# Kernel tuning notes

Measured on AMD Instinct MI355X. Metric: run time of the kernel, lower is better.

The kernel has to match this reference:

```python
import jax, jax.numpy as jnp
import numpy as np

NUM_HEADS = 8
DIM_HEAD = 40
SCALE = DIM_HEAD ** (-1.0 / 4.0)  # applied to q AND k, net 1/sqrt(dim_head)


def setup_inputs() -> dict:
    key = jax.random.key(0)
    ks = jax.random.split(key, 7)
    B, T, Dq = 16, 4096, 320
    S, Dc = 77, 768
    inner = NUM_HEADS * DIM_HEAD  # 320
    return {
        "x": jax.random.normal(ks[0], (B, T, Dq), jnp.float32),
        "context": jax.random.normal(ks[1], (B, S, Dc), jnp.float32),
        "Wq": jax.random.normal(ks[2], (Dq, inner), jnp.float32) * 0.02,
        "Wk": jax.random.normal(ks[3], (Dc, inner), jnp.float32) * 0.02,
        "Wv": jax.random.normal(ks[4], (Dc, inner), jnp.float32) * 0.02,
        "Wo": jax.random.normal(ks[5], (inner, Dq), jnp.float32) * 0.02,
        "bo": jnp.zeros((Dq,), jnp.float32),
    }


def reference(x, context, Wq, Wk, Wv, Wo, bo):
    B, T, _ = x.shape
    S = context.shape[1]
    H, C = NUM_HEADS, DIM_HEAD
    # projections; scale applied to q and k separately (dim_head^-1/4 each)
    q = (x @ Wq * SCALE).reshape(B, T, H, C)        # [B,T,H,C]
    k = (context @ Wk * SCALE).reshape(B, S, H, C)  # [B,S,H,C]
    v = (context @ Wv).reshape(B, S, H, C)          # [B,S,H,C]
    scores = jnp.einsum("bthc,bshc->bhts", q, k)    # [B,H,T,S]
    attn = jax.nn.softmax(scores, axis=-1)
    out = jnp.einsum("bhts,bshc->bthc", attn, v).reshape(B, T, H * C)
    return out @ Wo + bo
```

## Files before the change

### kernel.cpp

```cpp
#include <hip/hip_runtime.h>
#include <math.h>


#define NUM_HEADS 8
#define DIM_HEAD 40
#define INNER 320
#define DQ 320
#define DC 768
#define SEQ_T 4096
#define SEQ_S 77
#define BATCH 16
#define M_TOTAL (BATCH * SEQ_T)
#define MKV 1232
#define MKV_PAD 1280
#define SCALE 0.39763536438352531f

typedef __attribute__((ext_vector_type(8))) short short8;
typedef __attribute__((ext_vector_type(4))) float floatx4;

__device__ __forceinline__ unsigned short f2bf(float f) {
  unsigned u = __float_as_uint(f);
  u += 0x7FFFu + ((u >> 16) & 1u);
  return (unsigned short)(u >> 16);
}

#define CTXBLKS (MKV_PAD * DC / 8 / 256)
__global__ __launch_bounds__(256) void convert_ctx_kernel(
    const float* __restrict__ ctx, unsigned short* __restrict__ ctxb) {
  size_t t = (size_t)blockIdx.x * 256 + threadIdx.x;
  int row = (int)(t / (DC / 8)), col = (int)(t % (DC / 8)) * 8;
  int4 pk = make_int4(0, 0, 0, 0);
  if (row < MKV) {
    const float* p = &ctx[(size_t)row * DC + col];
    float4 a = *(const float4*)p, b = *(const float4*)(p + 4);
    pk.x = (int)(f2bf(a.x) | ((unsigned)f2bf(a.y) << 16));
    pk.y = (int)(f2bf(a.z) | ((unsigned)f2bf(a.w) << 16));
    pk.z = (int)(f2bf(b.x) | ((unsigned)f2bf(b.y) << 16));
    pk.w = (int)(f2bf(b.z) | ((unsigned)f2bf(b.w) << 16));
  }
  *(int4*)&ctxb[(size_t)row * DC + col] = pk;
}

__global__ __launch_bounds__(256) void transpose_w_kernel(
    const float* __restrict__ Wq, const float* __restrict__ Wo,
    const float* __restrict__ Wk, const float* __restrict__ Wv,
    unsigned short* __restrict__ WqT, unsigned short* __restrict__ WoT,
    unsigned short* __restrict__ WkvT) {
  const int z = blockIdx.z;
  const float* W; unsigned short* WT; int KD; float scl = 1.0f;
  if (z == 0)      { W = Wq; WT = WqT;  KD = 320; }
  else if (z == 1) { W = Wo; WT = WoT;  KD = 320; }
  else if (z == 2) { W = Wk; WT = WkvT; KD = DC; scl = SCALE; }
  else             { W = Wv; WT = WkvT + (size_t)INNER * DC; KD = DC; }
  const int k0 = blockIdx.x * 32;
  if (k0 >= KD) return;
  const int n0 = blockIdx.y * 32;
  __shared__ float tile[32][33];
  int tx = threadIdx.x & 31, ty = threadIdx.x >> 5;
  #pragma unroll
  for (int r = 0; r < 4; ++r)
    tile[ty + r * 8][tx] = W[(size_t)(k0 + ty + r * 8) * 320 + n0 + tx];
  __syncthreads();
  #pragma unroll
  for (int r = 0; r < 4; ++r)
    WT[(size_t)(n0 + ty + r * 8) * KD + k0 + tx] = f2bf(tile[tx][ty + r * 8] * scl);
}

#define GBM 128
#define GBN 160
#define GBK 64

template <bool OUT_BF16, int K, int CN>
__global__ __launch_bounds__(256) void gemm_mfma_kernel(
    const unsigned short* __restrict__ A, const unsigned short* __restrict__ B,
    void* __restrict__ C, const float* __restrict__ bias, float scale) {
  __shared__ __align__(16) unsigned short As[GBM * GBK];
  __shared__ __align__(16) unsigned short Bs[GBN * GBK];
  const int tid = threadIdx.x;
  const int lane = tid & 63, wave = tid >> 6;
  const int wm = (wave & 1) * 64, wn = (wave >> 1) * 80;
  const int lrow = lane & 15, quad = lane >> 4;
  const unsigned short* Ab = A + (size_t)blockIdx.x * GBM * K;
  const unsigned short* Bb = B + (size_t)blockIdx.y * GBN * K;

  floatx4 acc[4][5];
  #pragma unroll
  for (int i = 0; i < 4; ++i)
    #pragma unroll
    for (int j = 0; j < 5; ++j) acc[i][j] = (floatx4){0.f, 0.f, 0.f, 0.f};

  for (int kb = 0; kb < K / GBK; ++kb) {
    const int k0 = kb * GBK;
    #pragma unroll
    for (int rnd = 0; rnd < 4; ++rnd) {
      int off = rnd * 4096 + tid * 16;
      int m = off >> 7, cl = (off >> 4) & 7, cg = cl ^ (m & 7);
      __builtin_amdgcn_global_load_lds(
          (const __attribute__((address_space(1))) void*)(Ab + (size_t)m * K + k0 + cg * 8),
          (__attribute__((address_space(3))) void*)((char*)As + off), 16, 0, 0);
    }
    #pragma unroll
    for (int rnd = 0; rnd < 5; ++rnd) {
      int off = rnd * 4096 + tid * 16;
      int n = off >> 7, cl = (off >> 4) & 7, cg = cl ^ (n & 7);
      __builtin_amdgcn_global_load_lds(
          (const __attribute__((address_space(1))) void*)(Bb + (size_t)n * K + k0 + cg * 8),
          (__attribute__((address_space(3))) void*)((char*)Bs + off), 16, 0, 0);
    }
    __syncthreads();
    #pragma unroll
    for (int ks = 0; ks < 2; ++ks) {
      short8 fa[4], fb[5];
      #pragma unroll
      for (int i = 0; i < 4; ++i) {
        int m = wm + i * 16 + lrow;
        int cl = (ks * 4 + quad) ^ (m & 7);
        fa[i] = *(const short8*)&As[m * GBK + cl * 8];
      }
      #pragma unroll
      for (int j = 0; j < 5; ++j) {
        int n = wn + j * 16 + lrow;
        int cl = (ks * 4 + quad) ^ (n & 7);
        fb[j] = *(const short8*)&Bs[n * GBK + cl * 8];
      }
      #pragma unroll
      for (int i = 0; i < 4; ++i)
        #pragma unroll
        for (int j = 0; j < 5; ++j)
          acc[i][j] = __builtin_amdgcn_mfma_f32_16x16x32_bf16(fa[i], fb[j], acc[i][j], 0, 0, 0);
    }
    __syncthreads();
  }
  #pragma unroll
  for (int i = 0; i < 4; ++i)
    #pragma unroll
    for (int j = 0; j < 5; ++j) {
      int n = blockIdx.y * GBN + wn + j * 16 + lrow;
      float bv = bias ? bias[n] : 0.f;
      #pragma unroll
      for (int r = 0; r < 4; ++r) {
        size_t m = (size_t)blockIdx.x * GBM + wm + i * 16 + quad * 4 + r;
        float val = acc[i][j][r] * scale + bv;
        if (OUT_BF16) ((unsigned short*)C)[m * CN + n] = f2bf(val);
        else          ((float*)C)[m * CN + n] = val;
      }
    }
}

__global__ __launch_bounds__(256) void prep_kv_kernel(
    const float* __restrict__ kvw, unsigned short* __restrict__ kvp) {
  const int b = blockIdx.x >> 3, h = blockIdx.x & 7;
  unsigned short* dst = kvp + (size_t)blockIdx.x * 8192;
  const float* kvb = kvw + (size_t)b * SEQ_S * 640;
  for (int i = threadIdx.x; i < 3200; i += 256) {
    int s = i / 40, c = i % 40;
    unsigned short v = 0;
    if (s < SEQ_S) v = f2bf(kvb[(size_t)s * 640 + h * DIM_HEAD + c]);
    dst[i] = v;
  }
  for (int i = threadIdx.x; i < 4992; i += 256) {
    int c = i / 104, s = i % 104;
    unsigned short v = 0;
    if (s < SEQ_S && c < DIM_HEAD)
      v = f2bf(kvb[(size_t)s * 640 + 320 + h * DIM_HEAD + c]);
    dst[3200 + i] = v;
  }
}

#define QS_STRIDE 328
#define LDS_STAGE 41984

__global__ __launch_bounds__(512) void fused_attn_kernel(
    const float* __restrict__ x, const unsigned short* __restrict__ WqT,
    const unsigned short* __restrict__ kvp, const unsigned short* __restrict__ WoT,
    const float* __restrict__ bo, float* __restrict__ out) {
  __shared__ __align__(16) unsigned short lds[70656];
  unsigned short* qs = lds;
  unsigned short* As = lds + LDS_STAGE;
  unsigned short* Bs = lds + LDS_STAGE + 8192;
  const int tid = threadIdx.x;
  const int lane = tid & 63, wave = tid >> 6;
  const int lrow = lane & 15, quad = lane >> 4;
  const int b = blockIdx.x >> 5;
  const int t0 = (blockIdx.x & 31) * 128;
  const int wm = (wave & 1) * 64, wn = (wave >> 1) * 80;

  {
    const float* xb = x + ((size_t)b * SEQ_T + t0) * DQ;
    floatx4 acc[4][5];
    #pragma unroll
    for (int i = 0; i < 4; ++i)
      #pragma unroll
      for (int j = 0; j < 5; ++j) acc[i][j] = (floatx4){0.f, 0.f, 0.f, 0.f};
    for (int kb = 0; kb < 5; ++kb) {
      const int k0 = kb * 64;
      #pragma unroll
      for (int rnd = 0; rnd < 2; ++rnd) {
        int off = rnd * 8192 + tid * 16;
        int m = off >> 7, cl = (off >> 4) & 7, cg = cl ^ (m & 7);
        const float* src = xb + (size_t)m * DQ + k0 + cg * 8;
        float4 a = *(const float4*)src, c = *(const float4*)(src + 4);
        short8 pk;
        pk[0] = (short)f2bf(a.x); pk[1] = (short)f2bf(a.y);
        pk[2] = (short)f2bf(a.z); pk[3] = (short)f2bf(a.w);
        pk[4] = (short)f2bf(c.x); pk[5] = (short)f2bf(c.y);
        pk[6] = (short)f2bf(c.z); pk[7] = (short)f2bf(c.w);
        *(short8*)((char*)As + off) = pk;
      }
      #pragma unroll
      for (int rnd = 0; rnd < 5; ++rnd) {
        int off = rnd * 8192 + tid * 16;
        int n = off >> 7, cl = (off >> 4) & 7, cg = cl ^ (n & 7);
        __builtin_amdgcn_global_load_lds(
            (const __attribute__((address_space(1))) void*)(WqT + (size_t)n * 320 + k0 + cg * 8),
            (__attribute__((address_space(3))) void*)((char*)Bs + off), 16, 0, 0);
      }
      __syncthreads();
      #pragma unroll
      for (int ks = 0; ks < 2; ++ks) {
        short8 fa[4], fb[5];
        #pragma unroll
        for (int i = 0; i < 4; ++i) {
          int m = wm + i * 16 + lrow;
          int cl = (ks * 4 + quad) ^ (m & 7);
          fa[i] = *(const short8*)&As[m * 64 + cl * 8];
        }
        #pragma unroll
        for (int j = 0; j < 5; ++j) {
          int n = wn + j * 16 + lrow;
          int cl = (ks * 4 + quad) ^ (n & 7);
          fb[j] = *(const short8*)&Bs[n * 64 + cl * 8];
        }
        #pragma unroll
        for (int i = 0; i < 4; ++i)
          #pragma unroll
          for (int j = 0; j < 5; ++j)
            acc[i][j] = __builtin_amdgcn_mfma_f32_16x16x32_bf16(fa[i], fb[j], acc[i][j], 0, 0, 0);
      }
      __syncthreads();
    }
    #pragma unroll
    for (int i = 0; i < 4; ++i)
      #pragma unroll
      for (int j = 0; j < 5; ++j)
        #pragma unroll
        for (int r = 0; r < 4; ++r)
          qs[(wm + i * 16 + quad * 4 + r) * QS_STRIDE + wn + j * 16 + lrow] =
              f2bf(acc[i][j][r] * SCALE);
  }
  __syncthreads();

  {
    unsigned short* Kb = lds + LDS_STAGE;
    unsigned short* Vt = lds + LDS_STAGE + 3200;
    unsigned short* Pw = lds + LDS_STAGE + 8192 + wave * 1664;
    const short8 zero8 = {0, 0, 0, 0, 0, 0, 0, 0};
    for (int h = 0; h < NUM_HEADS; ++h) {
      const unsigned short* kvbh = kvp + (size_t)(b * NUM_HEADS + h) * 8192;
      #pragma unroll
      for (int rnd = 0; rnd < 2; ++rnd) {
        int off = rnd * 8192 + tid * 16;
        __builtin_amdgcn_global_load_lds(
            (const __attribute__((address_space(1))) void*)((const char*)kvbh + off),
            (__attribute__((address_space(3))) void*)((char*)Kb + off), 16, 0, 0);
      }
      __syncthreads();
      const int qrow = wave * 16 + lrow;
      short8 fq0 = *(const short8*)&qs[qrow * QS_STRIDE + h * DIM_HEAD + quad * 8];
      short8 fq1 = (quad == 0)
                       ? *(const short8*)&qs[qrow * QS_STRIDE + h * DIM_HEAD + 32]
                       : zero8;
      floatx4 sc[5];
      #pragma unroll
      for (int j = 0; j < 5; ++j) sc[j] = (floatx4){0.f, 0.f, 0.f, 0.f};
      #pragma unroll
      for (int j = 0; j < 5; ++j) {
        int srow = j * 16 + lrow;
        short8 fb0 = *(const short8*)&Kb[srow * 40 + quad * 8];
        short8 fb1 = *(const short8*)&Kb[srow * 40 + 32 + quad * 8];
        sc[j] = __builtin_amdgcn_mfma_f32_16x16x32_bf16(fq0, fb0, sc[j], 0, 0, 0);
        sc[j] = __builtin_amdgcn_mfma_f32_16x16x32_bf16(fq1, fb1, sc[j], 0, 0, 0);
      }
      float lsum[4] = {0.f, 0.f, 0.f, 0.f};
      #pragma unroll
      for (int j = 0; j < 5; ++j) {
        int s = j * 16 + lrow;
        #pragma unroll
        for (int r = 0; r < 4; ++r) {
          float p = (s < SEQ_S) ? __expf(sc[j][r]) : 0.f;
          Pw[(quad * 4 + r) * 104 + s] = f2bf(p);
          lsum[r] += p;
        }
      }
      #pragma unroll
      for (int r = 0; r < 4; ++r) Pw[(quad * 4 + r) * 104 + 80 + lrow] = 0;
      #pragma unroll
      for (int r = 0; r < 4; ++r) {
        float v = lsum[r];
        v += __shfl_xor(v, 1); v += __shfl_xor(v, 2);
        v += __shfl_xor(v, 4); v += __shfl_xor(v, 8);
        lsum[r] = 1.0f / v;
      }
      floatx4 oc[3];
      #pragma unroll
      for (int nj = 0; nj < 3; ++nj) oc[nj] = (floatx4){0.f, 0.f, 0.f, 0.f};
      #pragma unroll
      for (int ks = 0; ks < 3; ++ks) {
        short8 pa = *(const short8*)&Pw[lrow * 104 + ks * 32 + quad * 8];
        #pragma unroll
        for (int nj = 0; nj < 3; ++nj) {
          short8 vb = *(const short8*)&Vt[(nj * 16 + lrow) * 104 + ks * 32 + quad * 8];
          oc[nj] = __builtin_amdgcn_mfma_f32_16x16x32_bf16(pa, vb, oc[nj], 0, 0, 0);
        }
      }
      #pragma unroll
      for (int nj = 0; nj < 3; ++nj) {
        int c = nj * 16 + lrow;
        if (c < DIM_HEAD) {
          #pragma unroll
          for (int r = 0; r < 4; ++r)
            qs[(wave * 16 + quad * 4 + r) * QS_STRIDE + h * DIM_HEAD + c] =
                f2bf(oc[nj][r] * lsum[r]);
        }
      }
      __syncthreads();
    }
  }

  {
    floatx4 acc[4][5];
    #pragma unroll
    for (int i = 0; i < 4; ++i)
      #pragma unroll
      for (int j = 0; j < 5; ++j) acc[i][j] = (floatx4){0.f, 0.f, 0.f, 0.f};
    for (int kb = 0; kb < 5; ++kb) {
      const int k0 = kb * 64;
      #pragma unroll
      for (int rnd = 0; rnd < 5; ++rnd) {
        int off = rnd * 8192 + tid * 16;
        int n = off >> 7, cl = (off >> 4) & 7, cg = cl ^ (n & 7);
        __builtin_amdgcn_global_load_lds(
            (const __attribute__((address_space(1))) void*)(WoT + (size_t)n * 320 + k0 + cg * 8),
            (__attribute__((address_space(3))) void*)((char*)Bs + off), 16, 0, 0);
      }
      __syncthreads();
      #pragma unroll
      for (int ks = 0; ks < 2; ++ks) {
        short8 fa[4], fb[5];
        #pragma unroll
        for (int i = 0; i < 4; ++i)
          fa[i] = *(const short8*)&qs[(wm + i * 16 + lrow) * QS_STRIDE + k0 + ks * 32 + quad * 8];
        #pragma unroll
        for (int j = 0; j < 5; ++j) {
          int n = wn + j * 16 + lrow;
          int cl = (ks * 4 + quad) ^ (n & 7);
          fb[j] = *(const short8*)&Bs[n * 64 + cl * 8];
        }
        #pragma unroll
        for (int i = 0; i < 4; ++i)
          #pragma unroll
          for (int j = 0; j < 5; ++j)
            acc[i][j] = __builtin_amdgcn_mfma_f32_16x16x32_bf16(fa[i], fb[j], acc[i][j], 0, 0, 0);
      }
      __syncthreads();
    }
    float* ob = out + ((size_t)b * SEQ_T + t0) * DQ;
    #pragma unroll
    for (int i = 0; i < 4; ++i)
      #pragma unroll
      for (int j = 0; j < 5; ++j) {
        int n = wn + j * 16 + lrow;
        float bv = bo[n];
        #pragma unroll
        for (int r = 0; r < 4; ++r)
          ob[(size_t)(wm + i * 16 + quad * 4 + r) * DQ + n] = acc[i][j][r] + bv;
      }
  }
}

extern "C" void kernel_launch(void* const* d_in, const int* in_sizes, int n_in,
                              void* d_out, int out_size, void* d_ws, size_t ws_size,
                              hipStream_t stream) {
  const float* x   = (const float*)d_in[0];
  const float* ctx = (const float*)d_in[1];
  const float* Wq  = (const float*)d_in[2];
  const float* Wk  = (const float*)d_in[3];
  const float* Wv  = (const float*)d_in[4];
  const float* Wo  = (const float*)d_in[5];
  const float* bo  = (const float*)d_in[6];
  float* out = (float*)d_out;

  char* w = (char*)d_ws;
  unsigned short* ctxb = (unsigned short*)(w);
  unsigned short* WkvT = (unsigned short*)(w + 1966080);
  float*          kvw  = (float*)(w + 2949120);
  unsigned short* WqT  = (unsigned short*)(w + 6225920);
  unsigned short* WoT  = (unsigned short*)(w + 6430720);
  unsigned short* kvp  = (unsigned short*)(w + 6635520);

  hipLaunchKernelGGL(convert_ctx_kernel, dim3(CTXBLKS), dim3(256), 0, stream, ctx, ctxb);
  hipLaunchKernelGGL(transpose_w_kernel, dim3(24, 10, 4), dim3(256), 0, stream,
                     Wq, Wo, Wk, Wv, WqT, WoT, WkvT);
  hipLaunchKernelGGL((gemm_mfma_kernel<false, DC, 640>), dim3(MKV_PAD / GBM, 640 / GBN),
                     dim3(256), 0, stream, ctxb, WkvT, (void*)kvw, (const float*)nullptr, 1.0f);
  hipLaunchKernelGGL(prep_kv_kernel, dim3(BATCH * NUM_HEADS), dim3(256), 0, stream, kvw, kvp);
  hipLaunchKernelGGL(fused_attn_kernel, dim3(BATCH * (SEQ_T / 128)), dim3(512), 0, stream,
                     x, WqT, kvp, WoT, bo, out);
}
```

Measured before the change: 255.6 us.

## Shrink fused attention tiles to 64 rows and fuse KV packing into GEMM

The fused attention kernel now uses 64-row tiles with 256 threads and BK=32, which cuts LDS use roughly in half so more blocks can be resident per CU. The x tile is loaded one step ahead in registers before conversion to bf16. The KV projection GEMM now writes bf16 straight into the per-head packed K/V layout, so the fp32 intermediate buffer and the separate prep_kv pass are gone. A memset is added to zero the padding. Smaller tiles mean each block reuses the weight tiles across fewer rows and has to synchronise more often.

```diff
diff --git a/kernel.cpp b/kernel.cpp
--- a/kernel.cpp
+++ b/kernel.cpp
@@ -70,18 +70,17 @@
 #define GBN 160
 #define GBK 64
 
-template <bool OUT_BF16, int K, int CN>
-__global__ __launch_bounds__(256) void gemm_mfma_kernel(
+__global__ __launch_bounds__(256) void gemm_kv_pack_kernel(
     const unsigned short* __restrict__ A, const unsigned short* __restrict__ B,
-    void* __restrict__ C, const float* __restrict__ bias, float scale) {
+    unsigned short* __restrict__ kvp) {
   __shared__ __align__(16) unsigned short As[GBM * GBK];
   __shared__ __align__(16) unsigned short Bs[GBN * GBK];
   const int tid = threadIdx.x;
   const int lane = tid & 63, wave = tid >> 6;
   const int wm = (wave & 1) * 64, wn = (wave >> 1) * 80;
   const int lrow = lane & 15, quad = lane >> 4;
-  const unsigned short* Ab = A + (size_t)blockIdx.x * GBM * K;
-  const unsigned short* Bb = B + (size_t)blockIdx.y * GBN * K;
+  const unsigned short* Ab = A + (size_t)blockIdx.x * GBM * DC;
+  const unsigned short* Bb = B + (size_t)blockIdx.y * GBN * DC;
 
   floatx4 acc[4][5];
   #pragma unroll
@@ -89,14 +88,14 @@
     #pragma unroll
     for (int j = 0; j < 5; ++j) acc[i][j] = (floatx4){0.f, 0.f, 0.f, 0.f};
 
-  for (int kb = 0; kb < K / GBK; ++kb) {
+  for (int kb = 0; kb < DC / GBK; ++kb) {
     const int k0 = kb * GBK;
     #pragma unroll
     for (int rnd = 0; rnd < 4; ++rnd) {
       int off = rnd * 4096 + tid * 16;
       int m = off >> 7, cl = (off >> 4) & 7, cg = cl ^ (m & 7);
       __builtin_amdgcn_global_load_lds(
-          (const __attribute__((address_space(1))) void*)(Ab + (size_t)m * K + k0 + cg * 8),
+          (const __attribute__((address_space(1))) void*)(Ab + (size_t)m * DC + k0 + cg * 8),
           (__attribute__((address_space(3))) void*)((char*)As + off), 16, 0, 0);
     }
     #pragma unroll
@@ -104,7 +103,7 @@
       int off = rnd * 4096 + tid * 16;
       int n = off >> 7, cl = (off >> 4) & 7, cg = cl ^ (n & 7);
       __builtin_amdgcn_global_load_lds(
-          (const __attribute__((address_space(1))) void*)(Bb + (size_t)n * K + k0 + cg * 8),
+          (const __attribute__((address_space(1))) void*)(Bb + (size_t)n * DC + k0 + cg * 8),
           (__attribute__((address_space(3))) void*)((char*)Bs + off), 16, 0, 0);
     }
     __syncthreads();
@@ -136,108 +135,100 @@
     #pragma unroll
     for (int j = 0; j < 5; ++j) {
       int n = blockIdx.y * GBN + wn + j * 16 + lrow;
-      float bv = bias ? bias[n] : 0.f;
       #pragma unroll
       for (int r = 0; r < 4; ++r) {
-        size_t m = (size_t)blockIdx.x * GBM + wm + i * 16 + quad * 4 + r;
-        float val = acc[i][j][r] * scale + bv;
-        if (OUT_BF16) ((unsigned short*)C)[m * CN + n] = f2bf(val);
-        else          ((float*)C)[m * CN + n] = val;
-      }
-    }
-}
-
-__global__ __launch_bounds__(256) void prep_kv_kernel(
-    const float* __restrict__ kvw, unsigned short* __restrict__ kvp) {
-  const int b = blockIdx.x >> 3, h = blockIdx.x & 7;
-  unsigned short* dst = kvp + (size_t)blockIdx.x * 8192;
-  const float* kvb = kvw + (size_t)b * SEQ_S * 640;
-  for (int i = threadIdx.x; i < 3200; i += 256) {
-    int s = i / 40, c = i % 40;
-    unsigned short v = 0;
-    if (s < SEQ_S) v = f2bf(kvb[(size_t)s * 640 + h * DIM_HEAD + c]);
-    dst[i] = v;
-  }
-  for (int i = threadIdx.x; i < 4992; i += 256) {
-    int c = i / 104, s = i % 104;
-    unsigned short v = 0;
-    if (s < SEQ_S && c < DIM_HEAD)
-      v = f2bf(kvb[(size_t)s * 640 + 320 + h * DIM_HEAD + c]);
-    dst[3200 + i] = v;
-  }
+        int m = blockIdx.x * GBM + wm + i * 16 + quad * 4 + r;
+        if (m < MKV) {
+          unsigned um = (unsigned)m;
+          int b = (int)(um / 77u), s = (int)(um - (unsigned)b * 77u);
+          unsigned short* base = kvp + (size_t)b * (NUM_HEADS * 8192);
+          unsigned short v = f2bf(acc[i][j][r]);
+          if (n < 320) {
+            unsigned un = (unsigned)n;
+            int h = (int)(un / 40u), c = (int)(un - (unsigned)h * 40u);
+            base[(size_t)h * 8192 + s * 40 + c] = v;
+          } else {
+            unsigned un = (unsigned)(n - 320);
+            int h = (int)(un / 40u), c = (int)(un - (unsigned)h * 40u);
+            base[(size_t)h * 8192 + 3200 + c * 104 + s] = v;
+          }
+        }
+      }
+    }
 }
 
 #define QS_STRIDE 328
-#define LDS_STAGE 41984
-
-__global__ __launch_bounds__(512) void fused_attn_kernel(
+#define S0 20992
+
+__global__ __launch_bounds__(256) void fused_attn_kernel(
     const float* __restrict__ x, const unsigned short* __restrict__ WqT,
     const unsigned short* __restrict__ kvp, const unsigned short* __restrict__ WoT,
     const float* __restrict__ bo, float* __restrict__ out) {
-  __shared__ __align__(16) unsigned short lds[70656];
+  __shared__ __align__(16) unsigned short lds[35840];
   unsigned short* qs = lds;
-  unsigned short* As = lds + LDS_STAGE;
-  unsigned short* Bs = lds + LDS_STAGE + 8192;
   const int tid = threadIdx.x;
   const int lane = tid & 63, wave = tid >> 6;
   const int lrow = lane & 15, quad = lane >> 4;
-  const int b = blockIdx.x >> 5;
-  const int t0 = (blockIdx.x & 31) * 128;
-  const int wm = (wave & 1) * 64, wn = (wave >> 1) * 80;
+  const int b = blockIdx.x >> 6;
+  const int t0 = (blockIdx.x & 63) * 64;
+  const int wn = wave * 80;
 
   {
+    unsigned short* As = lds + S0;
+    unsigned short* Bs = lds + S0 + 2048;
     const float* xb = x + ((size_t)b * SEQ_T + t0) * DQ;
     floatx4 acc[4][5];
     #pragma unroll
     for (int i = 0; i < 4; ++i)
       #pragma unroll
       for (int j = 0; j < 5; ++j) acc[i][j] = (floatx4){0.f, 0.f, 0.f, 0.f};
-    for (int kb = 0; kb < 5; ++kb) {
-      const int k0 = kb * 64;
-      #pragma unroll
-      for (int rnd = 0; rnd < 2; ++rnd) {
-        int off = rnd * 8192 + tid * 16;
-        int m = off >> 7, cl = (off >> 4) & 7, cg = cl ^ (m & 7);
-        const float* src = xb + (size_t)m * DQ + k0 + cg * 8;
-        float4 a = *(const float4*)src, c = *(const float4*)(src + 4);
-        short8 pk;
-        pk[0] = (short)f2bf(a.x); pk[1] = (short)f2bf(a.y);
-        pk[2] = (short)f2bf(a.z); pk[3] = (short)f2bf(a.w);
-        pk[4] = (short)f2bf(c.x); pk[5] = (short)f2bf(c.y);
-        pk[6] = (short)f2bf(c.z); pk[7] = (short)f2bf(c.w);
-        *(short8*)((char*)As + off) = pk;
-      }
+
+    const int soff = tid * 16;
+    const int sm = soff >> 6;
+    const int scl = (soff >> 4) & 3;
+    const int scg = scl ^ (sm & 3);
+    const float* xsrc = xb + (size_t)sm * DQ + scg * 8;
+    float4 xa = *(const float4*)xsrc, xc = *(const float4*)(xsrc + 4);
+
+    for (int kb = 0; kb < 10; ++kb) {
+      float4 na, nc;
+      if (kb < 9) {
+        const float* s = xsrc + (size_t)(kb + 1) * 32;
+        na = *(const float4*)s; nc = *(const float4*)(s + 4);
+      }
+      short8 pk;
+      pk[0] = (short)f2bf(xa.x); pk[1] = (short)f2bf(xa.y);
+      pk[2] = (short)f2bf(xa.z); pk[3] = (short)f2bf(xa.w);
+      pk[4] = (short)f2bf(xc.x); pk[5] = (short)f2bf(xc.y);
+      pk[6] = (short)f2bf(xc.z); pk[7] = (short)f2bf(xc.w);
+      *(short8*)((char*)As + soff) = pk;
       #pragma unroll
       for (int rnd = 0; rnd < 5; ++rnd) {
-        int off = rnd * 8192 + tid * 16;
-        int n = off >> 7, cl = (off >> 4) & 7, cg = cl ^ (n & 7);
+        int off = rnd * 4096 + tid * 16;
+        int n = off >> 6, cl = (off >> 4) & 3, cg = cl ^ (n & 3);
         __builtin_amdgcn_global_load_lds(
-            (const __attribute__((address_space(1))) void*)(WqT + (size_t)n * 320 + k0 + cg * 8),
+            (const __attribute__((address_space(1))) void*)(WqT + (size_t)n * 320 + kb * 32 + cg * 8),
             (__attribute__((address_space(3))) void*)((char*)Bs + off), 16, 0, 0);
       }
       __syncthreads();
-      #pragma unroll
-      for (int ks = 0; ks < 2; ++ks) {
-        short8 fa[4], fb[5];
-        #pragma unroll
-        for (int i = 0; i < 4; ++i) {
-          int m = wm + i * 16 + lrow;
-          int cl = (ks * 4 + quad) ^ (m & 7);
-          fa[i] = *(const short8*)&As[m * 64 + cl * 8];
-        }
-        #pragma unroll
-        for (int j = 0; j < 5; ++j) {
-          int n = wn + j * 16 + lrow;
-          int cl = (ks * 4 + quad) ^ (n & 7);
-          fb[j] = *(const short8*)&Bs[n * 64 + cl * 8];
-        }
-        #pragma unroll
-        for (int i = 0; i < 4; ++i)
-          #pragma unroll
-          for (int j = 0; j < 5; ++j)
-            acc[i][j] = __builtin_amdgcn_mfma_f32_16x16x32_bf16(fa[i], fb[j], acc[i][j], 0, 0, 0);
-      }
-      __syncthreads();
+      short8 fa[4], fb[5];
+      #pragma unroll
+      for (int i = 0; i < 4; ++i) {
+        int m = i * 16 + lrow;
+        fa[i] = *(const short8*)&As[m * 32 + ((quad ^ (m & 3)) * 8)];
+      }
+      #pragma unroll
+      for (int j = 0; j < 5; ++j) {
+        int n = wn + j * 16 + lrow;
+        fb[j] = *(const short8*)&Bs[n * 32 + ((quad ^ (n & 3)) * 8)];
+      }
+      #pragma unroll
+      for (int i = 0; i < 4; ++i)
+        #pragma unroll
+        for (int j = 0; j < 5; ++j)
+          acc[i][j] = __builtin_amdgcn_mfma_f32_16x16x32_bf16(fa[i], fb[j], acc[i][j], 0, 0, 0);
+      __syncthreads();
+      if (kb < 9) { xa = na; xc = nc; }
     }
     #pragma unroll
     for (int i = 0; i < 4; ++i)
@@ -245,21 +236,21 @@
       for (int j = 0; j < 5; ++j)
         #pragma unroll
         for (int r = 0; r < 4; ++r)
-          qs[(wm + i * 16 + quad * 4 + r) * QS_STRIDE + wn + j * 16 + lrow] =
+          qs[(i * 16 + quad * 4 + r) * QS_STRIDE + wn + j * 16 + lrow] =
               f2bf(acc[i][j][r] * SCALE);
   }
   __syncthreads();
 
   {
-    unsigned short* Kb = lds + LDS_STAGE;
-    unsigned short* Vt = lds + LDS_STAGE + 3200;
-    unsigned short* Pw = lds + LDS_STAGE + 8192 + wave * 1664;
+    unsigned short* Kb = lds + S0;
+    unsigned short* Vt = lds + S0 + 3200;
+    unsigned short* Pw = lds + S0 + 8192 + wave * 1664;
     const short8 zero8 = {0, 0, 0, 0, 0, 0, 0, 0};
     for (int h = 0; h < NUM_HEADS; ++h) {
       const unsigned short* kvbh = kvp + (size_t)(b * NUM_HEADS + h) * 8192;
       #pragma unroll
-      for (int rnd = 0; rnd < 2; ++rnd) {
-        int off = rnd * 8192 + tid * 16;
+      for (int rnd = 0; rnd < 4; ++rnd) {
+        int off = rnd * 4096 + tid * 16;
         __builtin_amdgcn_global_load_lds(
             (const __attribute__((address_space(1))) void*)((const char*)kvbh + off),
             (__attribute__((address_space(3))) void*)((char*)Kb + off), 16, 0, 0);
@@ -328,40 +319,36 @@
   }
 
   {
+    unsigned short* Bs = lds + S0;
     floatx4 acc[4][5];
     #pragma unroll
     for (int i = 0; i < 4; ++i)
       #pragma unroll
       for (int j = 0; j < 5; ++j) acc[i][j] = (floatx4){0.f, 0.f, 0.f, 0.f};
-    for (int kb = 0; kb < 5; ++kb) {
-      const int k0 = kb * 64;
+    for (int kb = 0; kb < 10; ++kb) {
       #pragma unroll
       for (int rnd = 0; rnd < 5; ++rnd) {
-        int off = rnd * 8192 + tid * 16;
-        int n = off >> 7, cl = (off >> 4) & 7, cg = cl ^ (n & 7);
+        int off = rnd * 4096 + tid * 16;
+        int n = off >> 6, cl = (off >> 4) & 3, cg = cl ^ (n & 3);
         __builtin_amdgcn_global_load_lds(
-            (const __attribute__((address_space(1))) void*)(WoT + (size_t)n * 320 + k0 + cg * 8),
+            (const __attribute__((address_space(1))) void*)(WoT + (size_t)n * 320 + kb * 32 + cg * 8),
             (__attribute__((address_space(3))) void*)((char*)Bs + off), 16, 0, 0);
       }
       __syncthreads();
-      #pragma unroll
-      for (int ks = 0; ks < 2; ++ks) {
-        short8 fa[4], fb[5];
-        #pragma unroll
-        for (int i = 0; i < 4; ++i)
-          fa[i] = *(const short8*)&qs[(wm + i * 16 + lrow) * QS_STRIDE + k0 + ks * 32 + quad * 8];
-        #pragma unroll
-        for (int j = 0; j < 5; ++j) {
-          int n = wn + j * 16 + lrow;
-          int cl = (ks * 4 + quad) ^ (n & 7);
-          fb[j] = *(const short8*)&Bs[n * 64 + cl * 8];
-        }
-        #pragma unroll
-        for (int i = 0; i < 4; ++i)
-          #pragma unroll
-          for (int j = 0; j < 5; ++j)
-            acc[i][j] = __builtin_amdgcn_mfma_f32_16x16x32_bf16(fa[i], fb[j], acc[i][j], 0, 0, 0);
-      }
+      short8 fa[4], fb[5];
+      #pragma unroll
+      for (int i = 0; i < 4; ++i)
+        fa[i] = *(const short8*)&qs[(i * 16 + lrow) * QS_STRIDE + kb * 32 + quad * 8];
+      #pragma unroll
+      for (int j = 0; j < 5; ++j) {
+        int n = wn + j * 16 + lrow;
+        fb[j] = *(const short8*)&Bs[n * 32 + ((quad ^ (n & 3)) * 8)];
+      }
+      #pragma unroll
+      for (int i = 0; i < 4; ++i)
+        #pragma unroll
+        for (int j = 0; j < 5; ++j)
+          acc[i][j] = __builtin_amdgcn_mfma_f32_16x16x32_bf16(fa[i], fb[j], acc[i][j], 0, 0, 0);
       __syncthreads();
     }
     float* ob = out + ((size_t)b * SEQ_T + t0) * DQ;
@@ -373,7 +360,7 @@
         float bv = bo[n];
         #pragma unroll
         for (int r = 0; r < 4; ++r)
-          ob[(size_t)(wm + i * 16 + quad * 4 + r) * DQ + n] = acc[i][j][r] + bv;
+          ob[(size_t)(i * 16 + quad * 4 + r) * DQ + n] = acc[i][j][r] + bv;
       }
   }
 }
@@ -393,17 +380,16 @@
   char* w = (char*)d_ws;
   unsigned short* ctxb = (unsigned short*)(w);
   unsigned short* WkvT = (unsigned short*)(w + 1966080);
-  float*          kvw  = (float*)(w + 2949120);
-  unsigned short* WqT  = (unsigned short*)(w + 6225920);
-  unsigned short* WoT  = (unsigned short*)(w + 6430720);
-  unsigned short* kvp  = (unsigned short*)(w + 6635520);
-
+  unsigned short* WqT  = (unsigned short*)(w + 2949120);
+  unsigned short* WoT  = (unsigned short*)(w + 3153920);
+  unsigned short* kvp  = (unsigned short*)(w + 3358720);
+
+  hipMemsetAsync(kvp, 0, 2097152, stream);
   hipLaunchKernelGGL(convert_ctx_kernel, dim3(CTXBLKS), dim3(256), 0, stream, ctx, ctxb);
   hipLaunchKernelGGL(transpose_w_kernel, dim3(24, 10, 4), dim3(256), 0, stream,
                      Wq, Wo, Wk, Wv, WqT, WoT, WkvT);
-  hipLaunchKernelGGL((gemm_mfma_kernel<false, DC, 640>), dim3(MKV_PAD / GBM, 640 / GBN),
-                     dim3(256), 0, stream, ctxb, WkvT, (void*)kvw, (const float*)nullptr, 1.0f);
-  hipLaunchKernelGGL(prep_kv_kernel, dim3(BATCH * NUM_HEADS), dim3(256), 0, stream, kvw, kvp);
-  hipLaunchKernelGGL(fused_attn_kernel, dim3(BATCH * (SEQ_T / 128)), dim3(512), 0, stream,
+  hipLaunchKernelGGL(gemm_kv_pack_kernel, dim3(MKV_PAD / GBM, 640 / GBN),
+                     dim3(256), 0, stream, ctxb, WkvT, kvp);
+  hipLaunchKernelGGL(fused_attn_kernel, dim3(BATCH * (SEQ_T / 64)), dim3(256), 0, stream,
                      x, WqT, kvp, WoT, bo, out);
 }
```

New measurement: 314.5 us. +23.1%, slower.
